# Kernel optimization log

Measured on AMD Instinct MI355X. Metric: run time of the kernel, lower is better.

## Reference

```python
import jax, jax.numpy as jnp
import numpy as np
from jax import lax

DIM = 256
SEQ = 1024
BATCH = 4
EPS = 1e-6
P_TANH_SCALE = 10.0


def setup_inputs() -> dict:
    key = jax.random.key(0)
    ks = jax.random.split(key, 12)
    d, n, b = DIM, SEQ, BATCH
    half = d // 2
    x = jax.random.normal(ks[0], (b, n, d), jnp.float32)
    # RoPE frequencies (standard llama-style), complex freqs_cis split into cos/sin
    inv_freq = 1.0 / (10000.0 ** (np.arange(half, dtype=np.float64) * 2.0 / d))
    ang = np.outer(np.arange(n, dtype=np.float64), inv_freq)  # (n, d/2)
    freqs_cis_cos = jnp.asarray(np.cos(ang), jnp.float32)
    freqs_cis_sin = jnp.asarray(np.sin(ang), jnp.float32)
    s = 1.0 / np.sqrt(d)
    Wqkv = jax.random.normal(ks[1], (3 * d, d), jnp.float32) * s
    qconv_w = jax.random.normal(ks[2], (d, 4), jnp.float32) * 0.3
    qconv_b = jax.random.normal(ks[3], (d,), jnp.float32) * 0.02
    kconv_w = jax.random.normal(ks[4], (d, 4), jnp.float32) * 0.3
    kconv_b = jax.random.normal(ks[5], (d,), jnp.float32) * 0.02
    vconv_w = jax.random.normal(ks[6], (d, 4), jnp.float32) * 0.3
    vconv_b = jax.random.normal(ks[7], (d,), jnp.float32) * 0.02
    Wparam = jax.random.normal(ks[8], (2, d), jnp.float32) * s
    bparam = jnp.zeros((2,), jnp.float32)
    W0 = jnp.eye(d, dtype=jnp.float32)  # nn.init.eye_
    Wgate = jax.random.normal(ks[9], (d, d), jnp.float32) * s
    Wout = jax.random.normal(ks[10], (d, d), jnp.float32) * s
    return dict(x=x, freqs_cis_cos=freqs_cis_cos, freqs_cis_sin=freqs_cis_sin,
                Wqkv=Wqkv, qconv_w=qconv_w, qconv_b=qconv_b,
                kconv_w=kconv_w, kconv_b=kconv_b, vconv_w=vconv_w, vconv_b=vconv_b,
                Wparam=Wparam, bparam=bparam, W0=W0, Wgate=Wgate, Wout=Wout)


def _causal_dwconv(x, w, bias):
    # x: (b,n,d); w: (d,4); torch Conv1d(k=4, pad=3, groups=d) truncated to [:n]
    # y[t] = sum_j w[:,j] * x[t-3+j]  (zero left-pad)
    b, n, d = x.shape
    xp = jnp.pad(x, ((0, 0), (3, 0), (0, 0)))
    y = sum(xp[:, j:j + n, :] * w[None, None, :, j] for j in range(4))
    return y + bias[None, None, :]


def _rope(x, cos, sin):
    # x: (b,n,d); pairs (x[...,2i], x[...,2i+1]) rotated by freqs_cis
    xr, xi = x[..., 0::2], x[..., 1::2]
    c, s = cos[None], sin[None]
    outr = xr * c - xi * s
    outi = xr * s + xi * c
    return jnp.stack((outr, outi), axis=-1).reshape(x.shape)


def _l2norm(x):
    nrm = jnp.linalg.norm(x, axis=-1, keepdims=True)
    return x / jnp.maximum(nrm, 1e-12)


def _forward(x, cos, sin, Wqkv, qw, qb, kw, kb, vw, vb, Wparam, bparam, W0, Wgate, Wout):
    b, n, d = x.shape
    qkv = x @ Wqkv.T
    q, k, v = jnp.split(qkv, 3, axis=-1)
    q = _causal_dwconv(q, qw, qb)
    k = _causal_dwconv(k, kw, kb)
    v = _causal_dwconv(v, vw, vb)
    q = _l2norm(_rope(q, cos, sin))
    k = _l2norm(_rope(k, cos, sin))
    params = x @ Wparam.T + bparam  # (b,n,2)
    eta = jax.nn.sigmoid(params[..., 0])    # (b,n)
    alpha = jax.nn.sigmoid(params[..., 1])  # (b,n)

    def step(carry, inp):
        A, W = carry                      # (b,d,d)
        qt, kt, vt, et, at = inp          # (b,d)x3, (b,)x2
        pred = jnp.einsum('bd,bde->be', kt, W)
        diff = pred - vt
        grad_pred = 3.0 * jnp.tanh(P_TANH_SCALE * diff) * (diff * diff)  # p == 3
        grad_W = kt[:, :, None] * grad_pred[:, None, :]
        A = at[:, None, None] * A - et[:, None, None] * grad_W
        a4 = jnp.square(jnp.square(A))  # q == 4
        denom = jnp.sqrt(a4.sum(axis=(-2, -1), keepdims=True)) + EPS
        W = A / denom
        yt = jnp.einsum('bd,bde->be', qt, W)
        return (A, W), yt

    A0 = jnp.zeros((b, d, d), x.dtype)
    W_init = jnp.broadcast_to(W0, (b, d, d)).astype(x.dtype)
    xs = (q.transpose(1, 0, 2), k.transpose(1, 0, 2), v.transpose(1, 0, 2),
          eta.T, alpha.T)
    _, yT = lax.scan(jax.checkpoint(step), (A0, W_init), xs)
    y = yT.transpose(1, 0, 2)  # (b,n,d)
    return (y @ Wout.T) * jax.nn.sigmoid(x @ Wgate.T)


def reference(x, freqs_cis_cos, freqs_cis_sin, Wqkv, qconv_w, qconv_b,
              kconv_w, kconv_b, vconv_w, vconv_b, Wparam, bparam, W0, Wgate, Wout):
    return _forward(x, freqs_cis_cos, freqs_cis_sin, Wqkv, qconv_w, qconv_b,
                    kconv_w, kconv_b, vconv_w, vconv_b, Wparam, bparam, W0, Wgate, Wout)
```

## Files before the change

kernel.cpp:

```cpp
#include <hip/hip_runtime.h>

#define DIMD 256
#define SEQT 1024
#define NB   4
#define KSTRIDE 272

typedef float v2f __attribute__((ext_vector_type(2)));
#define FMA2(a,b,c) __builtin_elementwise_fma((a),(b),(c))

__device__ __forceinline__ float sigmoidf_(float x){ return 1.0f/(1.0f+expf(-x)); }

template<int EPI>
__global__ __launch_bounds__(256) void gemm_bt(const float* __restrict__ A,
    const float* __restrict__ Bm, float* __restrict__ C, int N,
    const float* __restrict__ gpre)
{
  __shared__ float sA[64][68];
  __shared__ float sB[64][68];
  const int nb = N >> 6;
  const int bm = blockIdx.x / nb, bn = blockIdx.x - bm*nb;
  const int m0 = bm << 6, n0 = bn << 6;
  const int tid = threadIdx.x;
  const int tr = tid >> 4, tc = tid & 15;
  float acc[4][4];
  #pragma unroll
  for (int i=0;i<4;i++)
    #pragma unroll
    for (int j=0;j<4;j++) acc[i][j]=0.f;

  for (int kc=0;kc<4;kc++){
    __syncthreads();
    for (int i=tid;i<1024;i+=256){
      int r = i >> 4, q4 = i & 15;
      *(float4*)&sA[r][q4*4] = ((const float4*)(A  + (m0+r)*256 + kc*64))[q4];
      *(float4*)&sB[r][q4*4] = ((const float4*)(Bm + (n0+r)*256 + kc*64))[q4];
    }
    __syncthreads();
    #pragma unroll
    for (int kq=0;kq<16;kq++){
      float4 av[4], bv[4];
      #pragma unroll
      for (int i=0;i<4;i++) av[i] = *(const float4*)&sA[tr+16*i][kq*4];
      #pragma unroll
      for (int j=0;j<4;j++) bv[j] = *(const float4*)&sB[tc+16*j][kq*4];
      #pragma unroll
      for (int i=0;i<4;i++)
        #pragma unroll
        for (int j=0;j<4;j++)
          acc[i][j] = fmaf(av[i].x,bv[j].x, fmaf(av[i].y,bv[j].y,
                      fmaf(av[i].z,bv[j].z, fmaf(av[i].w,bv[j].w, acc[i][j]))));
    }
  }
  #pragma unroll
  for (int i=0;i<4;i++){
    #pragma unroll
    for (int j=0;j<4;j++){
      int m = m0 + tr + 16*i, n = n0 + tc + 16*j;
      float val = acc[i][j];
      if (EPI==1) val *= sigmoidf_(gpre[m*N+n]);
      C[m*N+n] = val;
    }
  }
}

__global__ __launch_bounds__(256) void prep_kernel(
    const float* __restrict__ qkvr, const float* __restrict__ x,
    const float* __restrict__ cosT, const float* __restrict__ sinT,
    const float* __restrict__ qw, const float* __restrict__ qbias,
    const float* __restrict__ kw, const float* __restrict__ kbias,
    const float* __restrict__ vw, const float* __restrict__ vbias,
    const float* __restrict__ Wparam, const float* __restrict__ bparam,
    float* __restrict__ qo, float* __restrict__ ko, float* __restrict__ vo,
    float* __restrict__ eo, float* __restrict__ ao)
{
  const int bt = blockIdx.x;
  const int t = bt & 1023;
  const int d = threadIdx.x;

  float4 wq = ((const float4*)qw)[d];
  float4 wk = ((const float4*)kw)[d];
  float4 wv = ((const float4*)vw)[d];
  const float wqj[4] = {wq.x,wq.y,wq.z,wq.w};
  const float wkj[4] = {wk.x,wk.y,wk.z,wk.w};
  const float wvj[4] = {wv.x,wv.y,wv.z,wv.w};
  float qa = qbias[d], ka = kbias[d], va = vbias[d];
  #pragma unroll
  for (int j=0;j<4;j++){
    int tt = t - 3 + j;
    if (tt >= 0) {
      const float* row = qkvr + (size_t)(bt - 3 + j) * 768;
      qa = fmaf(row[d],      wqj[j], qa);
      ka = fmaf(row[256+d],  wkj[j], ka);
      va = fmaf(row[512+d],  wvj[j], va);
    }
  }
  vo[bt*256 + d] = va;

  __shared__ float sq[256], sk[256];
  __shared__ float red[4][4];
  sq[d] = qa; sk[d] = ka;
  __syncthreads();
  const int i = d >> 1;
  const float c = cosT[t*128 + i], s = sinT[t*128 + i];
  float qr, krp;
  if ((d & 1) == 0) { qr = sq[d]*c - sq[d+1]*s;  krp = sk[d]*c - sk[d+1]*s; }
  else              { qr = sq[d-1]*s + sq[d]*c;  krp = sk[d-1]*s + sk[d]*c; }

  const float xd = x[bt*256 + d];
  float r0 = qr*qr, r1 = krp*krp, r2 = xd*Wparam[d], r3 = xd*Wparam[256+d];
  #pragma unroll
  for (int m=1;m<64;m<<=1){
    r0 += __shfl_xor(r0, m, 64);
    r1 += __shfl_xor(r1, m, 64);
    r2 += __shfl_xor(r2, m, 64);
    r3 += __shfl_xor(r3, m, 64);
  }
  const int w = d >> 6;
  if ((d & 63) == 0){ red[w][0]=r0; red[w][1]=r1; red[w][2]=r2; red[w][3]=r3; }
  __syncthreads();
  float qss = red[0][0]+red[1][0]+red[2][0]+red[3][0];
  float kss = red[0][1]+red[1][1]+red[2][1]+red[3][1];
  qo[bt*256+d] = qr  / fmaxf(sqrtf(qss), 1e-12f);
  ko[bt*256+d] = krp / fmaxf(sqrtf(kss), 1e-12f);
  if (d == 0){
    float p0 = red[0][2]+red[1][2]+red[2][2]+red[3][2] + bparam[0];
    float p1 = red[0][3]+red[1][3]+red[2][3]+red[3][3] + bparam[1];
    eo[bt] = 1.f/(1.f+expf(-p0));
    ao[bt] = 1.f/(1.f+expf(-p1));
  }
}

__global__ __launch_bounds__(1024, 4) void scan_kernel(
    const float* __restrict__ qn, const float* __restrict__ kn,
    const float* __restrict__ vn, const float* __restrict__ eta,
    const float* __restrict__ alpha, const float* __restrict__ W0,
    float* __restrict__ y)
{
  const int b = blockIdx.x;
  const int tid = threadIdx.x;
  const int rg = tid & 3;
  const int c  = tid >> 2;
  const int r0 = rg << 6;
  const int koff = 68 * rg;

  __shared__ float s_k[3][KSTRIDE], s_q[3][KSTRIDE], s_v[3][256];
  __shared__ float s_ea[3][2];
  __shared__ float s_s4[2][16];

  v2f A2[32];
  #pragma unroll
  for (int j=0;j<32;j++) A2[j] = (v2f)(0.f);

  const float* kb = kn + b*SEQT*DIMD;
  const float* qb = qn + b*SEQT*DIMD;
  const float* vb = vn + b*SEQT*DIMD;
  const float* eb = eta   + b*SEQT;
  const float* ab = alpha + b*SEQT;
  float* yb = y + b*SEQT*DIMD;

  if (tid < 64) {
    float4 v0 = ((const float4*)kb)[tid];
    *(float4*)&s_k[0][4*tid + (tid>>4)*4] = v0;
  } else if (tid < 128) {
    int i = tid-64;
    float4 v0 = ((const float4*)qb)[i];
    *(float4*)&s_q[0][4*i + (i>>4)*4] = v0;
  } else if (tid < 192) {
    ((float4*)s_v[0])[tid-128] = ((const float4*)vb)[tid-128];
  }
  if (tid == 192) { s_ea[0][0] = eb[0]; s_ea[0][1] = ab[0]; }

  float4 pf = make_float4(0.f,0.f,0.f,0.f);
  float pe = 0.f, pa = 0.f;
  if (tid < 64)       pf = ((const float4*)(kb + DIMD))[tid];
  else if (tid < 128) pf = ((const float4*)(qb + DIMD))[tid-64];
  else if (tid < 192) pf = ((const float4*)(vb + DIMD))[tid-128];
  if (tid == 192) { pe = eb[1]; pa = ab[1]; }
  __syncthreads();

  float inv_prev = 1.0f;
  float u_prev = 0.f;
  int cur = 0;

  for (int t=0; t<SEQT; ++t) {
    const int nxt = (cur==2) ? 0 : cur+1;

    if (t+1 < SEQT) {
      if (tid < 64)       *(float4*)&s_k[nxt][4*tid + (tid>>4)*4] = pf;
      else if (tid < 128){ int i = tid-64; *(float4*)&s_q[nxt][4*i + (i>>4)*4] = pf; }
      else if (tid < 192) ((float4*)s_v[nxt])[tid-128] = pf;
      if (tid == 192) { s_ea[nxt][0]=pe; s_ea[nxt][1]=pa; }
    }

    float pred_raw;
    if (t == 0) {
      const float* w0p = W0 + (size_t)r0*DIMD + c;
      const float* kq = s_k[0] + koff;
      float acc = 0.f;
      #pragma unroll
      for (int j=0;j<64;j++)
        acc = fmaf(kq[j], w0p[(size_t)j*DIMD], acc);
      pred_raw = acc;
    } else {
      const float4* kp = (const float4*)(s_k[cur] + koff);
      v2f acc0 = (v2f)(0.f), acc1 = (v2f)(0.f);
      #pragma unroll
      for (int jq=0;jq<16;jq++){
        float4 kv = kp[jq];
        v2f klo = {kv.x, kv.y}, khi = {kv.z, kv.w};
        acc0 = FMA2(klo, A2[2*jq],   acc0);
        acc1 = FMA2(khi, A2[2*jq+1], acc1);
      }
      pred_raw = (acc0.x + acc0.y) + (acc1.x + acc1.y);
    }
    pred_raw += __shfl_xor(pred_raw, 1, 64);
    pred_raw += __shfl_xor(pred_raw, 2, 64);

    __syncthreads();

    if (t+2 < SEQT) {
      if (tid < 64)       pf = ((const float4*)(kb + (t+2)*DIMD))[tid];
      else if (tid < 128) pf = ((const float4*)(qb + (t+2)*DIMD))[tid-64];
      else if (tid < 192) pf = ((const float4*)(vb + (t+2)*DIMD))[tid-128];
      if (tid == 192) { pe = eb[t+2]; pa = ab[t+2]; }
    }

    if (t > 0) {
      const float* sp = s_s4[(t-1)&1];
      float4 sa = ((const float4*)sp)[0], sb4 = ((const float4*)sp)[1];
      float4 sc4= ((const float4*)sp)[2], sd4 = ((const float4*)sp)[3];
      float s4t = ((sa.x+sa.y)+(sa.z+sa.w)) + ((sb4.x+sb4.y)+(sb4.z+sb4.w))
                + ((sc4.x+sc4.y)+(sc4.z+sc4.w)) + ((sd4.x+sd4.y)+(sd4.z+sd4.w));
      float w = sqrtf(s4t) + 1e-6f;
      float r = __builtin_amdgcn_rcpf(w);
      r = r * (2.f - w*r);
      inv_prev = r;
      if (rg == 0) yb[(t-1)*DIMD + c] = u_prev * r;
    }

    float pred = pred_raw * inv_prev;
    const float et = s_ea[cur][0], al = s_ea[cur][1];
    float df = pred - s_v[cur][c];
    float e  = __expf(20.f*df);
    float th = 1.f - 2.f*__builtin_amdgcn_rcpf(e + 1.f);
    float t0 = et * 3.f * th * (df*df);

    const v2f alv = {al, al};
    const v2f nt0 = {-t0, -t0};
    v2f s4a = (v2f)(0.f), s4b = (v2f)(0.f);
    v2f u2a = (v2f)(0.f), u2b = (v2f)(0.f);
    {
      const float4* kp = (const float4*)(s_k[cur] + koff);
      const float4* qp = (const float4*)(s_q[cur] + koff);
      #pragma unroll
      for (int jq=0;jq<16;jq++){
        float4 kv = kp[jq], qv = qp[jq];
        v2f klo = {kv.x, kv.y}, khi = {kv.z, kv.w};
        v2f qlo = {qv.x, qv.y}, qhi = {qv.z, qv.w};
        v2f a, a2;
        a = FMA2(alv, A2[2*jq],   nt0*klo); A2[2*jq]   = a;
        a2 = a*a; s4a = FMA2(a2, a2, s4a);  u2a = FMA2(qlo, a, u2a);
        a = FMA2(alv, A2[2*jq+1], nt0*khi); A2[2*jq+1] = a;
        a2 = a*a; s4b = FMA2(a2, a2, s4b);  u2b = FMA2(qhi, a, u2b);
      }
    }
    float u = (u2a.x + u2a.y) + (u2b.x + u2b.y);
    u += __shfl_xor(u, 1, 64);
    u += __shfl_xor(u, 2, 64);
    u_prev = u;

    float s4 = (s4a.x + s4a.y) + (s4b.x + s4b.y);
    #pragma unroll
    for (int m=1;m<64;m<<=1) s4 += __shfl_xor(s4, m, 64);
    if ((tid & 63) == 0) s_s4[t&1][tid>>6] = s4;

    cur = nxt;
  }

  __syncthreads();
  {
    const float* sp = s_s4[1];
    float4 sa = ((const float4*)sp)[0], sb4 = ((const float4*)sp)[1];
    float4 sc4= ((const float4*)sp)[2], sd4 = ((const float4*)sp)[3];
    float s4t = ((sa.x+sa.y)+(sa.z+sa.w)) + ((sb4.x+sb4.y)+(sb4.z+sb4.w))
              + ((sc4.x+sc4.y)+(sc4.z+sc4.w)) + ((sd4.x+sd4.y)+(sd4.z+sd4.w));
    float w = sqrtf(s4t) + 1e-6f;
    float r = __builtin_amdgcn_rcpf(w);
    r = r * (2.f - w*r);
    if (rg == 0) yb[1023*DIMD + c] = u_prev * r;
  }
}

extern "C" void kernel_launch(void* const* d_in, const int* in_sizes, int n_in,
                              void* d_out, int out_size, void* d_ws, size_t ws_size,
                              hipStream_t stream)
{
  const float* x     = (const float*)d_in[0];
  const float* cosT  = (const float*)d_in[1];
  const float* sinT  = (const float*)d_in[2];
  const float* Wqkv  = (const float*)d_in[3];
  const float* qw    = (const float*)d_in[4];
  const float* qb    = (const float*)d_in[5];
  const float* kw    = (const float*)d_in[6];
  const float* kb    = (const float*)d_in[7];
  const float* vw    = (const float*)d_in[8];
  const float* vb    = (const float*)d_in[9];
  const float* Wparam= (const float*)d_in[10];
  const float* bparam= (const float*)d_in[11];
  const float* W0    = (const float*)d_in[12];
  const float* Wgate = (const float*)d_in[13];
  const float* Wout  = (const float*)d_in[14];
  float* out = (float*)d_out;

  float* ws    = (float*)d_ws;
  float* qkvr  = ws;
  float* qn    = qkvr + 4*1024*768;
  float* kn    = qn   + 4*1024*256;
  float* vn    = kn   + 4*1024*256;
  float* eta   = vn   + 4*1024*256;
  float* alpha = eta  + 4096;
  float* yv    = qkvr;
  float* tmpg  = qkvr + 1048576;

  gemm_bt<0><<<dim3(64*12), 256, 0, stream>>>(x, Wqkv, qkvr, 768, nullptr);
  prep_kernel<<<dim3(4096), 256, 0, stream>>>(qkvr, x, cosT, sinT,
      qw, qb, kw, kb, vw, vb, Wparam, bparam, qn, kn, vn, eta, alpha);
  scan_kernel<<<dim3(NB), 1024, 0, stream>>>(qn, kn, vn, eta, alpha, W0, yv);
  gemm_bt<0><<<dim3(64*4), 256, 0, stream>>>(x, Wgate, tmpg, 256, nullptr);
  gemm_bt<1><<<dim3(64*4), 256, 0, stream>>>(yv, Wout, out, 256, tmpg);
}
```

Baseline: 3.051 ms.

## Retile scan state to 16x4 per thread and fuse next-step prediction into update

Each thread of the sequential scan now owns a 16-row by 4-column tile of the state matrix instead of 64 rows of one column, which changes the shared-memory k/q layout and puts the reductions on 16-lane shuffle trees. The k·A product for the next timestep is computed inside the current update loop, using the already-staged next k row, so the separate prediction pass over the register state is removed. Exchanges: more shuffles per step (4 vector accumulators over 4 levels), four tanh evaluations per thread, and an extra shared read stream in the hot loop.

```diff
diff --git a/kernel.cpp b/kernel.cpp
--- a/kernel.cpp
+++ b/kernel.cpp
@@ -3,12 +3,16 @@
 #define DIMD 256
 #define SEQT 1024
 #define NB   4
-#define KSTRIDE 272
+#define KBS  20
 
 typedef float v2f __attribute__((ext_vector_type(2)));
 #define FMA2(a,b,c) __builtin_elementwise_fma((a),(b),(c))
 
 __device__ __forceinline__ float sigmoidf_(float x){ return 1.0f/(1.0f+expf(-x)); }
+
+__device__ __forceinline__ v2f shfl_xor_v2(v2f v, int m){
+  v2f r; r.x = __shfl_xor(v.x, m, 64); r.y = __shfl_xor(v.y, m, 64); return r;
+}
 
 template<int EPI>
 __global__ __launch_bounds__(256) void gemm_bt(const float* __restrict__ A,
@@ -138,12 +142,13 @@
 {
   const int b = blockIdx.x;
   const int tid = threadIdx.x;
-  const int rg = tid & 3;
-  const int c  = tid >> 2;
-  const int r0 = rg << 6;
-  const int koff = 68 * rg;
-
-  __shared__ float s_k[3][KSTRIDE], s_q[3][KSTRIDE], s_v[3][256];
+  const int rg = tid & 15;
+  const int cg = tid >> 4;
+  const int r0 = rg << 4;
+  const int c0 = cg << 2;
+  const int koff = KBS * rg;
+
+  __shared__ float s_k[3][16*KBS], s_q[3][16*KBS], s_v[3][256];
   __shared__ float s_ea[3][2];
   __shared__ float s_s4[2][16];
 
@@ -160,11 +165,11 @@
 
   if (tid < 64) {
     float4 v0 = ((const float4*)kb)[tid];
-    *(float4*)&s_k[0][4*tid + (tid>>4)*4] = v0;
+    *(float4*)&s_k[0][KBS*(tid>>2) + 4*(tid&3)] = v0;
   } else if (tid < 128) {
     int i = tid-64;
     float4 v0 = ((const float4*)qb)[i];
-    *(float4*)&s_q[0][4*i + (i>>4)*4] = v0;
+    *(float4*)&s_q[0][KBS*(i>>2) + 4*(i&3)] = v0;
   } else if (tid < 192) {
     ((float4*)s_v[0])[tid-128] = ((const float4*)vb)[tid-128];
   }
@@ -178,43 +183,42 @@
   if (tid == 192) { pe = eb[1]; pa = ab[1]; }
   __syncthreads();
 
-  float inv_prev = 1.0f;
-  float u_prev = 0.f;
+  v2f pr01 = (v2f)(0.f), pr23 = (v2f)(0.f);
+  {
+    const float4* kp0 = (const float4*)(s_k[0] + koff);
+    #pragma unroll
+    for (int j=0;j<4;j++){
+      float4 k4 = kp0[j];
+      #pragma unroll
+      for (int i=0;i<4;i++){
+        float ks = ((const float*)&k4)[i];
+        v2f ksv = {ks, ks};
+        int r = r0 + 4*j + i;
+        float4 w4 = *(const float4*)(W0 + (size_t)r*DIMD + c0);
+        v2f w01 = {w4.x, w4.y}, w23 = {w4.z, w4.w};
+        pr01 = FMA2(ksv, w01, pr01);
+        pr23 = FMA2(ksv, w23, pr23);
+      }
+    }
+    #pragma unroll
+    for (int m=1;m<16;m<<=1){
+      pr01 += shfl_xor_v2(pr01, m);
+      pr23 += shfl_xor_v2(pr23, m);
+    }
+  }
+
+  v2f up01 = (v2f)(0.f), up23 = (v2f)(0.f);
   int cur = 0;
 
   for (int t=0; t<SEQT; ++t) {
     const int nxt = (cur==2) ? 0 : cur+1;
 
     if (t+1 < SEQT) {
-      if (tid < 64)       *(float4*)&s_k[nxt][4*tid + (tid>>4)*4] = pf;
-      else if (tid < 128){ int i = tid-64; *(float4*)&s_q[nxt][4*i + (i>>4)*4] = pf; }
+      if (tid < 64)       *(float4*)&s_k[nxt][KBS*(tid>>2) + 4*(tid&3)] = pf;
+      else if (tid < 128){ int i = tid-64; *(float4*)&s_q[nxt][KBS*(i>>2) + 4*(i&3)] = pf; }
       else if (tid < 192) ((float4*)s_v[nxt])[tid-128] = pf;
       if (tid == 192) { s_ea[nxt][0]=pe; s_ea[nxt][1]=pa; }
     }
-
-    float pred_raw;
-    if (t == 0) {
-      const float* w0p = W0 + (size_t)r0*DIMD + c;
-      const float* kq = s_k[0] + koff;
-      float acc = 0.f;
-      #pragma unroll
-      for (int j=0;j<64;j++)
-        acc = fmaf(kq[j], w0p[(size_t)j*DIMD], acc);
-      pred_raw = acc;
-    } else {
-      const float4* kp = (const float4*)(s_k[cur] + koff);
-      v2f acc0 = (v2f)(0.f), acc1 = (v2f)(0.f);
-      #pragma unroll
-      for (int jq=0;jq<16;jq++){
-        float4 kv = kp[jq];
-        v2f klo = {kv.x, kv.y}, khi = {kv.z, kv.w};
-        acc0 = FMA2(klo, A2[2*jq],   acc0);
-        acc1 = FMA2(khi, A2[2*jq+1], acc1);
-      }
-      pred_raw = (acc0.x + acc0.y) + (acc1.x + acc1.y);
-    }
-    pred_raw += __shfl_xor(pred_raw, 1, 64);
-    pred_raw += __shfl_xor(pred_raw, 2, 64);
 
     __syncthreads();
 
@@ -225,6 +229,7 @@
       if (tid == 192) { pe = eb[t+2]; pa = ab[t+2]; }
     }
 
+    float scale = 1.f;
     if (t > 0) {
       const float* sp = s_s4[(t-1)&1];
       float4 sa = ((const float4*)sp)[0], sb4 = ((const float4*)sp)[1];
@@ -234,40 +239,68 @@
       float w = sqrtf(s4t) + 1e-6f;
       float r = __builtin_amdgcn_rcpf(w);
       r = r * (2.f - w*r);
-      inv_prev = r;
-      if (rg == 0) yb[(t-1)*DIMD + c] = u_prev * r;
-    }
-
-    float pred = pred_raw * inv_prev;
+      scale = r;
+      if (rg == 0) {
+        float4 yo = make_float4(up01.x*r, up01.y*r, up23.x*r, up23.y*r);
+        *(float4*)(yb + (size_t)(t-1)*DIMD + c0) = yo;
+      }
+    }
+
+    v2f pred01 = pr01 * scale, pred23 = pr23 * scale;
     const float et = s_ea[cur][0], al = s_ea[cur][1];
-    float df = pred - s_v[cur][c];
-    float e  = __expf(20.f*df);
-    float th = 1.f - 2.f*__builtin_amdgcn_rcpf(e + 1.f);
-    float t0 = et * 3.f * th * (df*df);
-
+    float4 v4 = *(const float4*)(s_v[cur] + c0);
+    v2f df01 = pred01 - (v2f){v4.x, v4.y};
+    v2f df23 = pred23 - (v2f){v4.z, v4.w};
+    float e0 = __expf(20.f*df01.x), e1 = __expf(20.f*df01.y);
+    float e2 = __expf(20.f*df23.x), e3 = __expf(20.f*df23.y);
+    v2f th01 = { 1.f - 2.f*__builtin_amdgcn_rcpf(e0+1.f),
+                 1.f - 2.f*__builtin_amdgcn_rcpf(e1+1.f) };
+    v2f th23 = { 1.f - 2.f*__builtin_amdgcn_rcpf(e2+1.f),
+                 1.f - 2.f*__builtin_amdgcn_rcpf(e3+1.f) };
+    const v2f etv = {et, et}, c3 = {3.f, 3.f};
+    v2f t0v01 = etv * c3 * th01 * (df01*df01);
+    v2f t0v23 = etv * c3 * th23 * (df23*df23);
     const v2f alv = {al, al};
-    const v2f nt0 = {-t0, -t0};
+
     v2f s4a = (v2f)(0.f), s4b = (v2f)(0.f);
-    v2f u2a = (v2f)(0.f), u2b = (v2f)(0.f);
+    v2f u01 = (v2f)(0.f), u23 = (v2f)(0.f);
+    v2f p01 = (v2f)(0.f), p23 = (v2f)(0.f);
     {
       const float4* kp = (const float4*)(s_k[cur] + koff);
       const float4* qp = (const float4*)(s_q[cur] + koff);
-      #pragma unroll
-      for (int jq=0;jq<16;jq++){
-        float4 kv = kp[jq], qv = qp[jq];
-        v2f klo = {kv.x, kv.y}, khi = {kv.z, kv.w};
-        v2f qlo = {qv.x, qv.y}, qhi = {qv.z, qv.w};
-        v2f a, a2;
-        a = FMA2(alv, A2[2*jq],   nt0*klo); A2[2*jq]   = a;
-        a2 = a*a; s4a = FMA2(a2, a2, s4a);  u2a = FMA2(qlo, a, u2a);
-        a = FMA2(alv, A2[2*jq+1], nt0*khi); A2[2*jq+1] = a;
-        a2 = a*a; s4b = FMA2(a2, a2, s4b);  u2b = FMA2(qhi, a, u2b);
+      const float4* np = (const float4*)(s_k[nxt] + koff);
+      #pragma unroll
+      for (int j=0;j<4;j++){
+        float4 k4 = kp[j], q4 = qp[j], n4 = np[j];
+        #pragma unroll
+        for (int i=0;i<4;i++){
+          float ks = ((const float*)&k4)[i];
+          float qs = ((const float*)&q4)[i];
+          float ns = ((const float*)&n4)[i];
+          v2f ksv = {ks,ks}, qsv = {qs,qs}, nsv = {ns,ns};
+          const int idx = 2*(4*j+i);
+          v2f a01 = FMA2(alv, A2[idx],   -(t0v01*ksv)); A2[idx]   = a01;
+          v2f a23 = FMA2(alv, A2[idx+1], -(t0v23*ksv)); A2[idx+1] = a23;
+          v2f sq01 = a01*a01, sq23 = a23*a23;
+          s4a = FMA2(sq01, sq01, s4a);
+          s4b = FMA2(sq23, sq23, s4b);
+          u01 = FMA2(qsv, a01, u01);
+          u23 = FMA2(qsv, a23, u23);
+          p01 = FMA2(nsv, a01, p01);
+          p23 = FMA2(nsv, a23, p23);
+        }
       }
     }
-    float u = (u2a.x + u2a.y) + (u2b.x + u2b.y);
-    u += __shfl_xor(u, 1, 64);
-    u += __shfl_xor(u, 2, 64);
-    u_prev = u;
+
+    #pragma unroll
+    for (int m=1;m<16;m<<=1){
+      p01 += shfl_xor_v2(p01, m);
+      p23 += shfl_xor_v2(p23, m);
+      u01 += shfl_xor_v2(u01, m);
+      u23 += shfl_xor_v2(u23, m);
+    }
+    pr01 = p01; pr23 = p23;
+    up01 = u01; up23 = u23;
 
     float s4 = (s4a.x + s4a.y) + (s4b.x + s4b.y);
     #pragma unroll
@@ -287,7 +320,10 @@
     float w = sqrtf(s4t) + 1e-6f;
     float r = __builtin_amdgcn_rcpf(w);
     r = r * (2.f - w*r);
-    if (rg == 0) yb[1023*DIMD + c] = u_prev * r;
+    if (rg == 0) {
+      float4 yo = make_float4(up01.x*r, up01.y*r, up23.x*r, up23.y*r);
+      *(float4*)(yb + (size_t)1023*DIMD + c0) = yo;
+    }
   }
 }
 
```

Measured after the change: 3.217 ms. 5.4% more time.

## Split scan state across two workgroups per batch with global sum-of-fourth-powers exchange

Applied to the files above, without the earlier changes.

Each batch's 256x256 recurrent state is now split by output column across two 1024-thread workgroups. Each thread holds 32 state entries instead of 64, which halves register pressure and per-step FMA work per workgroup. The normalization term is reduced within each workgroup through LDS atomics and exchanged with the peer workgroup through a global flag array, and the peer waits by spinning on acquire loads. The next step's prediction k·A is also fused into the update loop, which removes the separate matvec pass. In exchange, every step now pays a cross-CU handshake, and the design assumes both peer workgroups are resident at the same time.

```diff
diff --git a/kernel.cpp b/kernel.cpp
--- a/kernel.cpp
+++ b/kernel.cpp
@@ -3,7 +3,7 @@
 #define DIMD 256
 #define SEQT 1024
 #define NB   4
-#define KSTRIDE 272
+#define RBS  36
 
 typedef float v2f __attribute__((ext_vector_type(2)));
 #define FMA2(a,b,c) __builtin_elementwise_fma((a),(b),(c))
@@ -134,22 +134,27 @@
     const float* __restrict__ qn, const float* __restrict__ kn,
     const float* __restrict__ vn, const float* __restrict__ eta,
     const float* __restrict__ alpha, const float* __restrict__ W0,
-    float* __restrict__ y)
+    float* __restrict__ y, float* __restrict__ g_s4)
 {
-  const int b = blockIdx.x;
+  const int blkid = blockIdx.x;
+  const int b     = blkid >> 1;
+  const int h     = blkid & 1;
+  const int peerb = blkid ^ 1;
   const int tid = threadIdx.x;
-  const int rg = tid & 3;
-  const int c  = tid >> 2;
-  const int r0 = rg << 6;
-  const int koff = 68 * rg;
-
-  __shared__ float s_k[3][KSTRIDE], s_q[3][KSTRIDE], s_v[3][256];
+  const int rg = tid & 7;
+  const int cl = tid >> 3;
+  const int cg = (h << 7) + cl;
+  const int r0 = rg << 5;
+  const int koff = rg * RBS;
+
+  __shared__ float s_k[3][8*RBS], s_q[3][8*RBS], s_v[3][256];
   __shared__ float s_ea[3][2];
-  __shared__ float s_s4[2][16];
-
-  v2f A2[32];
-  #pragma unroll
-  for (int j=0;j<32;j++) A2[j] = (v2f)(0.f);
+  __shared__ float s_acc[4];
+  __shared__ unsigned s_cnt[4];
+
+  v2f A2[16];
+  #pragma unroll
+  for (int j=0;j<16;j++) A2[j] = (v2f)(0.f);
 
   const float* kb = kn + b*SEQT*DIMD;
   const float* qb = qn + b*SEQT*DIMD;
@@ -158,13 +163,15 @@
   const float* ab = alpha + b*SEQT;
   float* yb = y + b*SEQT*DIMD;
 
+  if (tid < 4) { s_acc[tid] = 0.f; s_cnt[tid] = 0u; }
+
   if (tid < 64) {
     float4 v0 = ((const float4*)kb)[tid];
-    *(float4*)&s_k[0][4*tid + (tid>>4)*4] = v0;
+    *(float4*)&s_k[0][(tid>>3)*RBS + (tid&7)*4] = v0;
   } else if (tid < 128) {
     int i = tid-64;
     float4 v0 = ((const float4*)qb)[i];
-    *(float4*)&s_q[0][4*i + (i>>4)*4] = v0;
+    *(float4*)&s_q[0][(i>>3)*RBS + (i&7)*4] = v0;
   } else if (tid < 192) {
     ((float4*)s_v[0])[tid-128] = ((const float4*)vb)[tid-128];
   }
@@ -178,45 +185,32 @@
   if (tid == 192) { pe = eb[1]; pa = ab[1]; }
   __syncthreads();
 
-  float inv_prev = 1.0f;
-  float u_prev = 0.f;
+  float pr = 0.f;
+  {
+    #pragma unroll 4
+    for (int j=0;j<32;j++)
+      pr = fmaf(s_k[0][koff + j], W0[(size_t)(r0+j)*DIMD + cg], pr);
+    pr += __shfl_xor(pr, 1, 64);
+    pr += __shfl_xor(pr, 2, 64);
+    pr += __shfl_xor(pr, 4, 64);
+  }
+
+  float up = 0.f;
   int cur = 0;
 
   for (int t=0; t<SEQT; ++t) {
     const int nxt = (cur==2) ? 0 : cur+1;
 
     if (t+1 < SEQT) {
-      if (tid < 64)       *(float4*)&s_k[nxt][4*tid + (tid>>4)*4] = pf;
-      else if (tid < 128){ int i = tid-64; *(float4*)&s_q[nxt][4*i + (i>>4)*4] = pf; }
+      if (tid < 64)       *(float4*)&s_k[nxt][(tid>>3)*RBS + (tid&7)*4] = pf;
+      else if (tid < 128){ int i = tid-64; *(float4*)&s_q[nxt][(i>>3)*RBS + (i&7)*4] = pf; }
       else if (tid < 192) ((float4*)s_v[nxt])[tid-128] = pf;
       if (tid == 192) { s_ea[nxt][0]=pe; s_ea[nxt][1]=pa; }
     }
 
-    float pred_raw;
-    if (t == 0) {
-      const float* w0p = W0 + (size_t)r0*DIMD + c;
-      const float* kq = s_k[0] + koff;
-      float acc = 0.f;
-      #pragma unroll
-      for (int j=0;j<64;j++)
-        acc = fmaf(kq[j], w0p[(size_t)j*DIMD], acc);
-      pred_raw = acc;
-    } else {
-      const float4* kp = (const float4*)(s_k[cur] + koff);
-      v2f acc0 = (v2f)(0.f), acc1 = (v2f)(0.f);
-      #pragma unroll
-      for (int jq=0;jq<16;jq++){
-        float4 kv = kp[jq];
-        v2f klo = {kv.x, kv.y}, khi = {kv.z, kv.w};
-        acc0 = FMA2(klo, A2[2*jq],   acc0);
-        acc1 = FMA2(khi, A2[2*jq+1], acc1);
-      }
-      pred_raw = (acc0.x + acc0.y) + (acc1.x + acc1.y);
-    }
-    pred_raw += __shfl_xor(pred_raw, 1, 64);
-    pred_raw += __shfl_xor(pred_raw, 2, 64);
-
     __syncthreads();
+
+    if (tid == 256) { s_acc[(t+1)&3] = 0.f; s_cnt[(t+1)&3] = 0u; }
 
     if (t+2 < SEQT) {
       if (tid < 64)       pf = ((const float4*)(kb + (t+2)*DIMD))[tid];
@@ -225,69 +219,89 @@
       if (tid == 192) { pe = eb[t+2]; pa = ab[t+2]; }
     }
 
+    float scale = 1.f;
     if (t > 0) {
-      const float* sp = s_s4[(t-1)&1];
-      float4 sa = ((const float4*)sp)[0], sb4 = ((const float4*)sp)[1];
-      float4 sc4= ((const float4*)sp)[2], sd4 = ((const float4*)sp)[3];
-      float s4t = ((sa.x+sa.y)+(sa.z+sa.w)) + ((sb4.x+sb4.y)+(sb4.z+sb4.w))
-                + ((sc4.x+sc4.y)+(sc4.z+sc4.w)) + ((sd4.x+sd4.y)+(sd4.z+sd4.w));
+      float own = s_acc[(t-1)&3];
+      const unsigned* pp = (const unsigned*)&g_s4[(size_t)(t-1)*8 + peerb];
+      unsigned pv;
+      do {
+        pv = __hip_atomic_load(pp, __ATOMIC_ACQUIRE, __HIP_MEMORY_SCOPE_AGENT);
+      } while (pv == 0xAAAAAAAAu);
+      float s4t = own + __uint_as_float(pv);
       float w = sqrtf(s4t) + 1e-6f;
       float r = __builtin_amdgcn_rcpf(w);
       r = r * (2.f - w*r);
-      inv_prev = r;
-      if (rg == 0) yb[(t-1)*DIMD + c] = u_prev * r;
-    }
-
-    float pred = pred_raw * inv_prev;
+      scale = r;
+      if (rg == 0) yb[(size_t)(t-1)*DIMD + cg] = up * r;
+    }
+
     const float et = s_ea[cur][0], al = s_ea[cur][1];
-    float df = pred - s_v[cur][c];
+    float pred = pr * scale;
+    float df = pred - s_v[cur][cg];
     float e  = __expf(20.f*df);
     float th = 1.f - 2.f*__builtin_amdgcn_rcpf(e + 1.f);
     float t0 = et * 3.f * th * (df*df);
-
-    const v2f alv = {al, al};
-    const v2f nt0 = {-t0, -t0};
-    v2f s4a = (v2f)(0.f), s4b = (v2f)(0.f);
-    v2f u2a = (v2f)(0.f), u2b = (v2f)(0.f);
-    {
-      const float4* kp = (const float4*)(s_k[cur] + koff);
-      const float4* qp = (const float4*)(s_q[cur] + koff);
-      #pragma unroll
-      for (int jq=0;jq<16;jq++){
-        float4 kv = kp[jq], qv = qp[jq];
-        v2f klo = {kv.x, kv.y}, khi = {kv.z, kv.w};
-        v2f qlo = {qv.x, qv.y}, qhi = {qv.z, qv.w};
-        v2f a, a2;
-        a = FMA2(alv, A2[2*jq],   nt0*klo); A2[2*jq]   = a;
-        a2 = a*a; s4a = FMA2(a2, a2, s4a);  u2a = FMA2(qlo, a, u2a);
-        a = FMA2(alv, A2[2*jq+1], nt0*khi); A2[2*jq+1] = a;
-        a2 = a*a; s4b = FMA2(a2, a2, s4b);  u2b = FMA2(qhi, a, u2b);
+    v2f nt0; nt0.x = -t0; nt0.y = -t0;
+    v2f alv; alv.x = al;  alv.y = al;
+
+    const float4* kp = (const float4*)(s_k[cur] + koff);
+    const float4* qp = (const float4*)(s_q[cur] + koff);
+    const float4* np = (const float4*)(s_k[nxt] + koff);
+    v2f s4v = (v2f)(0.f), uv = (v2f)(0.f), pv2 = (v2f)(0.f);
+    #pragma unroll
+    for (int j=0;j<8;j++){
+      float4 k4 = kp[j], q4 = qp[j], n4 = np[j];
+      v2f klo = {k4.x,k4.y}, khi = {k4.z,k4.w};
+      v2f qlo = {q4.x,q4.y}, qhi = {q4.z,q4.w};
+      v2f nlo = {n4.x,n4.y}, nhi = {n4.z,n4.w};
+      v2f a, sq;
+      a = FMA2(alv, A2[2*j],   nt0*klo); A2[2*j]   = a;
+      sq = a*a; s4v = FMA2(sq, sq, s4v);
+      uv  = FMA2(qlo, a, uv);
+      pv2 = FMA2(nlo, a, pv2);
+      a = FMA2(alv, A2[2*j+1], nt0*khi); A2[2*j+1] = a;
+      sq = a*a; s4v = FMA2(sq, sq, s4v);
+      uv  = FMA2(qhi, a, uv);
+      pv2 = FMA2(nhi, a, pv2);
+    }
+
+    float u = uv.x + uv.y;
+    float p = pv2.x + pv2.y;
+    u += __shfl_xor(u, 1, 64); p += __shfl_xor(p, 1, 64);
+    u += __shfl_xor(u, 2, 64); p += __shfl_xor(p, 2, 64);
+    u += __shfl_xor(u, 4, 64); p += __shfl_xor(p, 4, 64);
+    up = u; pr = p;
+
+    float s4 = s4v.x + s4v.y;
+    #pragma unroll
+    for (int m=1;m<64;m<<=1) s4 += __shfl_xor(s4, m, 64);
+    if ((tid & 63) == 0) {
+      atomicAdd(&s_acc[t&3], s4);
+      unsigned old = atomicAdd(&s_cnt[t&3], 1u);
+      if (old == 15u) {
+        float tot = s_acc[t&3];
+        __hip_atomic_store((unsigned*)&g_s4[(size_t)t*8 + blkid],
+                           __float_as_uint(tot),
+                           __ATOMIC_RELEASE, __HIP_MEMORY_SCOPE_AGENT);
       }
     }
-    float u = (u2a.x + u2a.y) + (u2b.x + u2b.y);
-    u += __shfl_xor(u, 1, 64);
-    u += __shfl_xor(u, 2, 64);
-    u_prev = u;
-
-    float s4 = (s4a.x + s4a.y) + (s4b.x + s4b.y);
-    #pragma unroll
-    for (int m=1;m<64;m<<=1) s4 += __shfl_xor(s4, m, 64);
-    if ((tid & 63) == 0) s_s4[t&1][tid>>6] = s4;
 
     cur = nxt;
   }
 
   __syncthreads();
   {
-    const float* sp = s_s4[1];
-    float4 sa = ((const float4*)sp)[0], sb4 = ((const float4*)sp)[1];
-    float4 sc4= ((const float4*)sp)[2], sd4 = ((const float4*)sp)[3];
-    float s4t = ((sa.x+sa.y)+(sa.z+sa.w)) + ((sb4.x+sb4.y)+(sb4.z+sb4.w))
-              + ((sc4.x+sc4.y)+(sc4.z+sc4.w)) + ((sd4.x+sd4.y)+(sd4.z+sd4.w));
+    float own = s_acc[1023&3];
+    const unsigned* pp = (const unsigned*)&g_s4[(size_t)1023*8 + peerb];
+    unsigned pv;
+    do {
+      pv = __hip_atomic_load(pp, __ATOMIC_ACQUIRE, __HIP_MEMORY_SCOPE_AGENT);
+    } while (pv == 0xAAAAAAAAu);
+    float s4t = own + __uint_as_float(pv);
     float w = sqrtf(s4t) + 1e-6f;
     float r = __builtin_amdgcn_rcpf(w);
     r = r * (2.f - w*r);
-    if (rg == 0) yb[1023*DIMD + c] = u_prev * r;
+    if (rg == 0) yb[(size_t)1023*DIMD + cg] = up * r;
   }
 }
 
@@ -321,11 +335,14 @@
   float* alpha = eta  + 4096;
   float* yv    = qkvr;
   float* tmpg  = qkvr + 1048576;
+  float* g_s4  = qkvr + 2097152;
 
   gemm_bt<0><<<dim3(64*12), 256, 0, stream>>>(x, Wqkv, qkvr, 768, nullptr);
   prep_kernel<<<dim3(4096), 256, 0, stream>>>(qkvr, x, cosT, sinT,
       qw, qb, kw, kb, vw, vb, Wparam, bparam, qn, kn, vn, eta, alpha);
-  scan_kernel<<<dim3(NB), 1024, 0, stream>>>(qn, kn, vn, eta, alpha, W0, yv);
+  hipMemsetAsync(g_s4, 0xAA, (size_t)SEQT*8*sizeof(float), stream);
+  scan_kernel<<<dim3(NB*2), 1024, 0, stream>>>(qn, kn, vn, eta, alpha, W0,
+                                               yv, g_s4);
   gemm_bt<0><<<dim3(64*4), 256, 0, stream>>>(x, Wgate, tmpg, 256, nullptr);
   gemm_bt<1><<<dim3(64*4), 256, 0, stream>>>(yv, Wout, out, 256, tmpg);
 }
```

Measured after the change: 3.131 ms. 1.03x slower.
